# Kernel tuning notes

Measured on AMD Instinct MI355X. Metric: run time of the kernel, lower is better.

Reference implementation:

```python
import jax, jax.numpy as jnp
import numpy as np

H, CM, CS = 8, 16, 32  # num_heads, hidden_mv_channels, hidden_s_channels
_INNER_IDX = np.array([0, 2, 3, 4, 8, 9, 10, 14])  # PGA multivector components without e0


def _make_basis():
    # 9 Pin(3,0,1)-equivariant linear maps on 16-dim multivectors:
    # 5 grade projections + 4 left-multiplications by e0 (grade k -> grade k+1 e0-blades).
    # Component order: [1, e0, e1, e2, e3, e01, e02, e03, e12, e13, e23, e012, e013, e023, e123, e0123]
    b = np.zeros((9, 16, 16), dtype=np.float32)
    grades = [[0], [1, 2, 3, 4], [5, 6, 7, 8, 9, 10], [11, 12, 13, 14], [15]]
    for k, idxs in enumerate(grades):
        for i in idxs:
            b[k, i, i] = 1.0
    e0maps = {5: [(0, 1)], 6: [(2, 5), (3, 6), (4, 7)], 7: [(8, 11), (9, 12), (10, 13)], 8: [(14, 15)]}
    for k, pairs in e0maps.items():
        for i, o in pairs:
            b[k, o, i] = 1.0
    return jnp.asarray(b)


BASIS = _make_basis()  # (9, 16_out_comp, 16_in_comp)


def equi_linear(mv, s, w_mv, w_s2mv, b_mv, w_mv2s, w_s2s, b_s):
    # mv: (..., c_in, 16); s: (..., s_in)
    out_mv = jnp.einsum('yai,ocy,...ci->...oa', BASIS, w_mv, mv)
    out_mv = out_mv.at[..., 0].add(jnp.einsum('...i,oi->...o', s, w_s2mv) + b_mv)
    out_s = (jnp.einsum('...c,sc->...s', mv[..., 0], w_mv2s)
             + jnp.einsum('...i,si->...s', s, w_s2s) + b_s)
    return out_mv, out_s


def reference(multivectors_kv, multivectors_q, scalars_kv, scalars_q,
              q_w_mv, q_w_s2mv, q_b_mv, q_w_mv2s, q_w_s2s, q_b_s,
              k_w_mv, k_w_s2mv, k_b_mv, k_w_mv2s, k_w_s2s, k_b_s,
              v_w_mv, v_w_s2mv, v_b_mv, v_w_mv2s, v_w_s2s, v_b_s,
              o_w_mv, o_w_s2mv, o_b_mv, o_w_mv2s, o_w_s2s, o_b_s):
    B, Q = multivectors_q.shape[0], multivectors_q.shape[1]
    q_mv, q_s = equi_linear(multivectors_q, scalars_q, q_w_mv, q_w_s2mv, q_b_mv, q_w_mv2s, q_w_s2s, q_b_s)
    k_mv, k_s = equi_linear(multivectors_kv, scalars_kv, k_w_mv, k_w_s2mv, k_b_mv, k_w_mv2s, k_w_s2s, k_b_s)
    v_mv, v_s = equi_linear(multivectors_kv, scalars_kv, v_w_mv, v_w_s2mv, v_b_mv, v_w_mv2s, v_w_s2s, v_b_s)
    # split heads; einops pattern '(hidden_channels num_heads)' => channel-major, head-minor
    q_mv = q_mv.reshape(B, Q, CM, H, 16).transpose(0, 3, 1, 2, 4)  # (B,H,Q,CM,16)
    q_s = q_s.reshape(B, Q, CS, H).transpose(0, 3, 1, 2)            # (B,H,Q,CS)
    # multi-query: single k/v head broadcast over H
    scale = 1.0 / jnp.sqrt(jnp.asarray(8 * CM + CS, dtype=q_mv.dtype))
    scores = (jnp.einsum('bhqcx,bkcx->bhqk', q_mv[..., _INNER_IDX], k_mv[..., _INNER_IDX])
              + jnp.einsum('bhqs,bks->bhqk', q_s, k_s)) * scale
    attn = jax.nn.softmax(scores, axis=-1)
    h_mv = jnp.einsum('bhqk,bkcx->bhqcx', attn, v_mv)
    h_s = jnp.einsum('bhqk,bkc->bhqc', attn, v_s)
    # merge heads; pattern '(n_heads hidden_channels)' => head-major
    h_mv = h_mv.transpose(0, 2, 1, 3, 4).reshape(B, Q, H * CM, 16)
    h_s = h_s.transpose(0, 2, 1, 3).reshape(B, Q, H * CS)
    out_mv, out_s = equi_linear(h_mv, h_s, o_w_mv, o_w_s2mv, o_b_mv, o_w_mv2s, o_w_s2s, o_b_s)
    return out_mv, out_s


def setup_inputs():
    key = jax.random.key(0)
    ks = jax.random.split(key, 32)
    B, NQ, NKV, IN_MV, IN_S = 4, 2048, 2048, 16, 32
    w = 0.05  # weight scale to keep attention logits sane

    def rn(k, shape, s=1.0):
        return jax.random.normal(k, shape, dtype=jnp.float32) * s

    return {
        'multivectors_kv': rn(ks[0], (B, NKV, IN_MV, 16)),
        'multivectors_q': rn(ks[1], (B, NQ, IN_MV, 16)),
        'scalars_kv': rn(ks[2], (B, NKV, IN_S)),
        'scalars_q': rn(ks[3], (B, NQ, IN_S)),
        'q_w_mv': rn(ks[4], (CM * H, IN_MV, 9), w),
        'q_w_s2mv': rn(ks[5], (CM * H, IN_S), w),
        'q_b_mv': jnp.zeros((CM * H,), jnp.float32),
        'q_w_mv2s': rn(ks[6], (CS * H, IN_MV), w),
        'q_w_s2s': rn(ks[7], (CS * H, IN_S), w),
        'q_b_s': jnp.zeros((CS * H,), jnp.float32),
        'k_w_mv': rn(ks[8], (CM, IN_MV, 9), w),
        'k_w_s2mv': rn(ks[9], (CM, IN_S), w),
        'k_b_mv': jnp.zeros((CM,), jnp.float32),
        'k_w_mv2s': rn(ks[10], (CS, IN_MV), w),
        'k_w_s2s': rn(ks[11], (CS, IN_S), w),
        'k_b_s': jnp.zeros((CS,), jnp.float32),
        'v_w_mv': rn(ks[12], (CM, IN_MV, 9), w),
        'v_w_s2mv': rn(ks[13], (CM, IN_S), w),
        'v_b_mv': jnp.zeros((CM,), jnp.float32),
        'v_w_mv2s': rn(ks[14], (CS, IN_MV), w),
        'v_w_s2s': rn(ks[15], (CS, IN_S), w),
        'v_b_s': jnp.zeros((CS,), jnp.float32),
        'o_w_mv': rn(ks[16], (16, CM * H, 9), w),
        'o_w_s2mv': rn(ks[17], (16, CS * H), w),
        'o_b_mv': jnp.zeros((16,), jnp.float32),
        'o_w_mv2s': rn(ks[18], (32, CM * H), w),
        'o_w_s2s': rn(ks[19], (32, CS * H), w),
        'o_b_s': jnp.zeros((32,), jnp.float32),
    }
```

## Files before the change

### kernel.cpp

```cpp
#include <hip/hip_runtime.h>
#include <hip/hip_bf16.h>
#include <math.h>

#define NB   4
#define NQL  2048
#define NKVL 2048
#define HN   8
#define DQK  160
#define DV   288
#define QT   256
#define KTL  64
#define KLP  168

#define SCALE 0.07905694150420949f

typedef __attribute__((ext_vector_type(8)))  short short8;
typedef __attribute__((ext_vector_type(4)))  float f32x4;
typedef __attribute__((ext_vector_type(16))) float f32x16;

__constant__ int c_grade[16] = {0,1,1,1,1,2,2,2,2,2,2,3,3,3,3,4};
__constant__ int c_inner[8]  = {0,2,3,4,8,9,10,14};
__constant__ int c_esrc[16]  = {-1,0,-1,-1,-1,2,3,4,-1,-1,-1,8,9,10,-1,14};
__constant__ int c_ey[16]    = {0,5,0,0,0,6,6,6,0,0,0,7,7,7,0,8};

__device__ __forceinline__ ushort f2bf(float v) {
  __hip_bfloat16 h = __float2bfloat16(v);
  union { __hip_bfloat16 b; ushort u; } cv; cv.b = h; return cv.u;
}

__device__ __forceinline__ void gload16(const void* g, void* l) {
  __builtin_amdgcn_global_load_lds(
      (const __attribute__((address_space(1))) unsigned int*)g,
      (__attribute__((address_space(3))) unsigned int*)l, 16, 0, 0);
}

#define KWMV   0
#define KS2MV  2304
#define KMV2S  2816
#define KS2S   3328
#define KBMV   4352
#define KBS    4368
#define VWMV   4400
#define VS2MV  6704
#define VMV2S  7216
#define VS2S   7728
#define VBMV   8752
#define VBS    8768
#define WLSZ   8800
#define XSTR   289
#define OSTR   456
#define KVPOS  8

__device__ __forceinline__ void kv_accum(const float* wL, const float* xL,
                                         int f, float acc[KVPOS]) {
  if (f < 160) {
    if (f < 128) {
      int c = f >> 3, a = c_inner[f & 7], y = c_grade[a];
      float bias = (a == 0) ? wL[KBMV + c] : 0.f;
#pragma unroll
      for (int p = 0; p < KVPOS; p++) acc[p] = bias;
      for (int ci = 0; ci < 16; ci++) {
        float w = wL[KWMV + (c*16 + ci)*9 + y];
#pragma unroll
        for (int p = 0; p < KVPOS; p++) acc[p] += w * xL[p*XSTR + ci*16 + a];
      }
      if (a == 0) {
        for (int i2 = 0; i2 < 32; i2++) {
          float w = wL[KS2MV + c*32 + i2];
#pragma unroll
          for (int p = 0; p < KVPOS; p++) acc[p] += w * xL[p*XSTR + 256 + i2];
        }
      }
    } else {
      int si = f - 128;
      float bias = wL[KBS + si];
#pragma unroll
      for (int p = 0; p < KVPOS; p++) acc[p] = bias;
      for (int ci = 0; ci < 16; ci++) {
        float w = wL[KMV2S + si*16 + ci];
#pragma unroll
        for (int p = 0; p < KVPOS; p++) acc[p] += w * xL[p*XSTR + ci*16];
      }
      for (int i2 = 0; i2 < 32; i2++) {
        float w = wL[KS2S + si*32 + i2];
#pragma unroll
        for (int p = 0; p < KVPOS; p++) acc[p] += w * xL[p*XSTR + 256 + i2];
      }
    }
  } else {
    int g = f - 160;
    if (g < 256) {
      int c = g >> 4, a = g & 15, y = c_grade[a];
      float bias = (a == 0) ? wL[VBMV + c] : 0.f;
#pragma unroll
      for (int p = 0; p < KVPOS; p++) acc[p] = bias;
      for (int ci = 0; ci < 16; ci++) {
        float w = wL[VWMV + (c*16 + ci)*9 + y];
#pragma unroll
        for (int p = 0; p < KVPOS; p++) acc[p] += w * xL[p*XSTR + ci*16 + a];
      }
      int sa = c_esrc[a];
      if (sa >= 0) {
        int ey = c_ey[a];
        for (int ci = 0; ci < 16; ci++) {
          float w = wL[VWMV + (c*16 + ci)*9 + ey];
#pragma unroll
          for (int p = 0; p < KVPOS; p++) acc[p] += w * xL[p*XSTR + ci*16 + sa];
        }
      }
      if (a == 0) {
        for (int i2 = 0; i2 < 32; i2++) {
          float w = wL[VS2MV + c*32 + i2];
#pragma unroll
          for (int p = 0; p < KVPOS; p++) acc[p] += w * xL[p*XSTR + 256 + i2];
        }
      }
    } else {
      int si = g - 256;
      float bias = wL[VBS + si];
#pragma unroll
      for (int p = 0; p < KVPOS; p++) acc[p] = bias;
      for (int ci = 0; ci < 16; ci++) {
        float w = wL[VMV2S + si*16 + ci];
#pragma unroll
        for (int p = 0; p < KVPOS; p++) acc[p] += w * xL[p*XSTR + ci*16];
      }
      for (int i2 = 0; i2 < 32; i2++) {
        float w = wL[VS2S + si*32 + i2];
#pragma unroll
        for (int p = 0; p < KVPOS; p++) acc[p] += w * xL[p*XSTR + 256 + i2];
      }
    }
  }
}

__global__ __launch_bounds__(256) void proj_kv_kernel(
    const float* __restrict__ mv_kv, const float* __restrict__ s_kv,
    const float* __restrict__ kw_mv, const float* __restrict__ kw_s2mv, const float* __restrict__ kb_mv,
    const float* __restrict__ kw_mv2s, const float* __restrict__ kw_s2s, const float* __restrict__ kb_s,
    const float* __restrict__ vw_mv, const float* __restrict__ vw_s2mv, const float* __restrict__ vb_mv,
    const float* __restrict__ vw_mv2s, const float* __restrict__ vw_s2s, const float* __restrict__ vb_s,
    ushort* __restrict__ Kf, ushort* __restrict__ VfT)
{
  __shared__ float wL[WLSZ];
  __shared__ float xL[KVPOS*XSTR];
  int t = threadIdx.x;
  for (int i = t; i < 2304; i += 256) wL[KWMV + i] = kw_mv[i];
  for (int i = t; i < 512;  i += 256) wL[KS2MV + i] = kw_s2mv[i];
  for (int i = t; i < 512;  i += 256) wL[KMV2S + i] = kw_mv2s[i];
  for (int i = t; i < 1024; i += 256) wL[KS2S + i] = kw_s2s[i];
  if (t < 16) wL[KBMV + t] = kb_mv[t];
  if (t < 32) wL[KBS + t] = kb_s[t];
  for (int i = t; i < 2304; i += 256) wL[VWMV + i] = vw_mv[i];
  for (int i = t; i < 512;  i += 256) wL[VS2MV + i] = vw_s2mv[i];
  for (int i = t; i < 512;  i += 256) wL[VMV2S + i] = vw_mv2s[i];
  for (int i = t; i < 1024; i += 256) wL[VS2S + i] = vw_s2s[i];
  if (t < 16) wL[VBMV + t] = vb_mv[t];
  if (t < 32) wL[VBS + t] = vb_s[t];

  int p0 = blockIdx.x * KVPOS;
  for (int i = t; i < KVPOS*256; i += 256) {
    int p = i >> 8, c = i & 255;
    xL[p*XSTR + c] = mv_kv[(size_t)(p0 + p)*256 + c];
  }
  if (t < KVPOS*32) {
    int p = t >> 5, c = t & 31;
    xL[p*XSTR + 256 + c] = s_kv[(size_t)(p0 + p)*32 + c];
  }
  __syncthreads();

  float acc0[KVPOS], acc1[KVPOS];
  kv_accum(wL, xL, t, acc0);
  if (t < 192) kv_accum(wL, xL, 256 + t, acc1);
  __syncthreads();

  ushort* oL = (ushort*)xL;
#pragma unroll
  for (int p = 0; p < KVPOS; p++) oL[p*OSTR + t] = f2bf(acc0[p]);
  if (t < 192) {
#pragma unroll
    for (int p = 0; p < KVPOS; p++) oL[p*OSTR + 256 + t] = f2bf(acc1[p]);
  }
  __syncthreads();

  int b = p0 >> 11, kv0 = p0 & 2047;
  for (int it = 0; it < 3; it++) {
    int j = t + it*256;
    if (j < KVPOS*80) {
      int p = j / 80, fp = j - p*80;
      uint u = (uint)oL[p*OSTR + 2*fp] | ((uint)oL[p*OSTR + 2*fp + 1] << 16);
      *(uint*)(Kf + (size_t)(p0 + p)*DQK + 2*fp) = u;
    }
  }
  for (int it = 0; it < 5; it++) {
    int j = t + it*256;
    if (j < DV*(KVPOS/2)) {
      int g = j >> 2, pp = j & 3;
      uint u = (uint)oL[(2*pp)*OSTR + 160 + g] | ((uint)oL[(2*pp+1)*OSTR + 160 + g] << 16);
      int kv = kv0 + 2*pp;
      int pos = (kv & ~63) + ((((kv >> 3) & 7) ^ (g & 7)) << 3) + (kv & 7);
      *(uint*)(VfT + ((size_t)b*DV + g)*NKVL + pos) = u;
    }
  }
}

#define OWT_SZ 34816
#define QWT_MV 0
#define QWT_S  20480
#define QBT    61440
#define QWT_SZ 62720
__global__ __launch_bounds__(256) void prep_w_kernel(
    const float* __restrict__ ow_mv, const float* __restrict__ ow_s2mv,
    const float* __restrict__ ow_mv2s, const float* __restrict__ ow_s2s,
    float* __restrict__ owT,
    const float* __restrict__ qw_mv, const float* __restrict__ qw_s2mv, const float* __restrict__ qb_mv,
    const float* __restrict__ qw_mv2s, const float* __restrict__ qw_s2s, const float* __restrict__ qb_s,
    float* __restrict__ qwT)
{
  int i = blockIdx.x*256 + threadIdx.x;
  if (i < OWT_SZ) {
    if (i < 18432) {
      int y = i / 2048, r = i & 2047, ch = r >> 4, o = r & 15;
      owT[i] = ow_mv[(size_t)(o*128 + ch)*9 + y];
    } else if (i < 22528) {
      int r = i - 18432, jj = r >> 4, o = r & 15;
      owT[i] = ow_s2mv[o*256 + jj];
    } else if (i < 26624) {
      int r = i - 22528, ch = r >> 5, si = r & 31;
      owT[i] = ow_mv2s[si*128 + ch];
    } else {
      int r = i - 26624, jj = r >> 5, si = r & 31;
      owT[i] = ow_s2s[si*256 + jj];
    }
    return;
  }
  int j = i - OWT_SZ;
  if (j >= QWT_SZ) return;
  if (j < QWT_S) {
    int ci = j / 1280, r = j - ci*1280, h = r / 160, f0 = r - h*160;
    float v;
    if (f0 < 128) {
      int c = f0 >> 3, a = c_inner[f0 & 7], y = c_grade[a];
      v = qw_mv[((c*HN + h)*16 + ci)*9 + y];
    } else {
      v = qw_mv2s[((f0 - 128)*HN + h)*16 + ci];
    }
    qwT[j] = v;
  } else if (j < QBT) {
    int k = j - QWT_S;
    int i2 = k / 1280, r = k - i2*1280, h = r / 160, f0 = r - h*160;
    float v;
    if (f0 < 128) {
      int c = f0 >> 3, a = c_inner[f0 & 7];
      v = (a == 0) ? qw_s2mv[(c*HN + h)*32 + i2] : 0.f;
    } else {
      v = qw_s2s[((f0 - 128)*HN + h)*32 + i2];
    }
    qwT[j] = v;
  } else {
    int r = j - QBT, h = r / 160, f0 = r - h*160;
    float v;
    if (f0 < 128) {
      int c = f0 >> 3, a = c_inner[f0 & 7];
      v = (a == 0) ? qb_mv[c*HN + h] : 0.f;
    } else {
      v = qb_s[(f0 - 128)*HN + h];
    }
    qwT[j] = v;
  }
}

#define QPOS 8
__global__ __launch_bounds__(320) void proj_q_kernel(
    const float* __restrict__ mv_q, const float* __restrict__ s_q,
    const float* __restrict__ qwT,
    ushort* __restrict__ Qf)
{
  __shared__ float xL[QPOS*XSTR];
  int t = threadIdx.x;
  int p0 = blockIdx.x * QPOS;
  for (int i = t; i < QPOS*256; i += 320) {
    int p = i >> 8, c = i & 255;
    xL[p*XSTR + c] = mv_q[(size_t)(p0 + p)*256 + c];
  }
  if (t < QPOS*32) {
    int p = t >> 5, c = t & 31;
    xL[p*XSTR + 256 + c] = s_q[(size_t)(p0 + p)*32 + c];
  }
  __syncthreads();

  int f0 = t % 160;
  int h0 = t / 160;
  int a = (f0 < 128) ? c_inner[f0 & 7] : 0;

  float acc[4][QPOS];
#pragma unroll
  for (int k = 0; k < 4; k++) {
    float bv = qwT[QBT + (h0 + 2*k)*160 + f0];
#pragma unroll
    for (int p = 0; p < QPOS; p++) acc[k][p] = bv;
  }
  for (int ci = 0; ci < 16; ci++) {
    float w0 = qwT[QWT_MV + (ci*HN + h0    )*160 + f0];
    float w1 = qwT[QWT_MV + (ci*HN + h0 + 2)*160 + f0];
    float w2 = qwT[QWT_MV + (ci*HN + h0 + 4)*160 + f0];
    float w3 = qwT[QWT_MV + (ci*HN + h0 + 6)*160 + f0];
#pragma unroll
    for (int p = 0; p < QPOS; p++) {
      float xv = xL[p*XSTR + ci*16 + a];
      acc[0][p] += w0*xv; acc[1][p] += w1*xv;
      acc[2][p] += w2*xv; acc[3][p] += w3*xv;
    }
  }
  for (int i2 = 0; i2 < 32; i2++) {
    float w0 = qwT[QWT_S + (i2*HN + h0    )*160 + f0];
    float w1 = qwT[QWT_S + (i2*HN + h0 + 2)*160 + f0];
    float w2 = qwT[QWT_S + (i2*HN + h0 + 4)*160 + f0];
    float w3 = qwT[QWT_S + (i2*HN + h0 + 6)*160 + f0];
#pragma unroll
    for (int p = 0; p < QPOS; p++) {
      float xv = xL[p*XSTR + 256 + i2];
      acc[0][p] += w0*xv; acc[1][p] += w1*xv;
      acc[2][p] += w2*xv; acc[3][p] += w3*xv;
    }
  }

  int b = p0 >> 11, q0 = p0 & 2047;
#pragma unroll
  for (int k = 0; k < 4; k++) {
    int h = h0 + 2*k;
    ushort* qdst = Qf + ((size_t)(b*HN + h)*NQL + q0)*DQK + f0;
#pragma unroll
    for (int p = 0; p < QPOS; p++)
      qdst[p*DQK] = f2bf(acc[k][p] * SCALE);
  }
}

__global__ __launch_bounds__(512, 2) void attn_kernel(
    const ushort* __restrict__ Kf,
    const ushort* __restrict__ VfT,
    const ushort* __restrict__ Qf,
    float* __restrict__ Hf)
{
  __shared__ ushort kL[2][KTL*KLP];
  __shared__ ushort vtL[2][DV*KTL];

  const int NT = NQL/QT;
  int bid = blockIdx.x;
  int swz = (bid & 7) * 32 + (bid >> 3);
  int bh = swz / NT;
  int qt = swz - bh*NT;
  int b = bh >> 3, h = bh & 7;
  int t = threadIdx.x, w = t >> 6, l = t & 63;
  int ql = l & 31, hb = l >> 5;

  const ushort* kb = Kf  + (size_t)b*NKVL*DQK;
  const ushort* vb = VfT + (size_t)b*DV*NKVL;

  const ushort* qrow = Qf + ((size_t)bh*NQL + (size_t)qt*QT + w*32 + ql)*DQK + hb*8;
  short8 qf[10];
#pragma unroll
  for (int ks = 0; ks < 10; ks++)
    qf[ks] = *(const short8*)(qrow + ks*16);

  f32x16 oA[9];
#pragma unroll
  for (int i = 0; i < 9; i++) oA[i] = (f32x16)(0.f);
  float m = -INFINITY, lsum = 0.f;

#define STAGE(KT, BUF) do {                                            \
    const ushort* kg_ = kb + (size_t)(KT)*KTL*DQK;                     \
    char* kd_ = (char*)&kL[BUF][0];                                    \
    for (int c_ = w; c_ < 21; c_ += 8) {                               \
      int off_ = c_*1024 + l*16;                                       \
      int row_ = off_ / 336;                                           \
      int bc_  = off_ - row_*336;                                      \
      const ushort* ga_ = kg_ + row_*DQK + ((bc_ < 320) ? (bc_ >> 1) : 0); \
      gload16(ga_, kd_ + c_*1024);                                     \
    }                                                                  \
    const ushort* vg_ = vb + (size_t)(KT)*KTL;                         \
    char* vd_ = (char*)&vtL[BUF][0];                                   \
    for (int c_ = w; c_ < 36; c_ += 8) {                               \
      int off_ = c_*1024 + l*16;                                       \
      int d_  = off_ >> 7;                                             \
      int bc_ = off_ & 127;                                            \
      const ushort* ga_ = vg_ + (size_t)d_*NKVL + (bc_ >> 1);          \
      gload16(ga_, vd_ + c_*1024);                                     \
    }                                                                  \
  } while (0)

  STAGE(0, 0);
  __syncthreads();

  for (int kt = 0; kt < NKVL/KTL; kt++) {
    int cur = kt & 1;
    if (kt + 1 < NKVL/KTL) STAGE(kt + 1, cur ^ 1);

    const ushort* kbuf  = &kL[cur][0];
    const ushort* vtbuf = &vtL[cur][0];

    f32x16 sA[2];
    __builtin_amdgcn_s_setprio(1);
#pragma unroll
    for (int kvb = 0; kvb < 2; kvb++) {
      sA[kvb] = (f32x16)(0.f);
      const ushort* krow = kbuf + (ql + 32*kvb)*KLP + hb*8;
#pragma unroll
      for (int ks = 0; ks < 10; ks++) {
        short8 kf = *(const short8*)(krow + ks*16);
        sA[kvb] = __builtin_amdgcn_mfma_f32_32x32x16_bf16(kf, qf[ks], sA[kvb], 0, 0, 0);
      }
    }
    __builtin_amdgcn_s_setprio(0);

    float tm = sA[0][0];
#pragma unroll
    for (int kvb = 0; kvb < 2; kvb++)
#pragma unroll
      for (int r = 0; r < 16; r++) tm = fmaxf(tm, sA[kvb][r]);
    tm = fmaxf(tm, __shfl_xor(tm, 32));
    if (!__all(tm - m <= 8.0f)) {
      float nm = fmaxf(m, tm);
      float ef = __expf(m - nm);
      lsum *= ef;
#pragma unroll
      for (int i = 0; i < 9; i++)
#pragma unroll
        for (int r = 0; r < 16; r++) oA[i][r] *= ef;
      m = nm;
    }
    float rs = 0.f;
#pragma unroll
    for (int kvb = 0; kvb < 2; kvb++)
#pragma unroll
      for (int r = 0; r < 16; r++) {
        float p = __expf(sA[kvb][r] - m);
        sA[kvb][r] = p;
        rs += p;
      }
    rs += __shfl_xor(rs, 32);
    lsum += rs;

    unsigned int pk[2][8];
#pragma unroll
    for (int kvb = 0; kvb < 2; kvb++)
#pragma unroll
      for (int k = 0; k < 8; k++) {
        unsigned int r_;
        asm("v_cvt_pk_bf16_f32 %0, %1, %2" : "=v"(r_) : "v"(sA[kvb][2*k]), "v"(sA[kvb][2*k+1]));
        pk[kvb][k] = r_;
      }

#pragma unroll
    for (int s = 0; s < 4; s++) {
      const int n0 = 2*s, n1 = 2*s + 1;
      unsigned int u[4];
#pragma unroll
      for (int p = 0; p < 4; p++) {
        unsigned int Xa = pk[n0 >> 2][(p & 1) + 2*(n0 & 3)];
        unsigned int Xb = pk[n1 >> 2][(p & 1) + 2*(n1 & 3)];
        int src = ql + 32*(p >> 1);
        unsigned int ua = __shfl((int)Xa, src);
        unsigned int ub = __shfl((int)Xb, src);
        u[p] = hb ? ub : ua;
      }
      union { unsigned int uu[4]; short8 s8; } pf;
      pf.uu[0] = u[0]; pf.uu[1] = u[1]; pf.uu[2] = u[2]; pf.uu[3] = u[3];
      __builtin_amdgcn_s_setprio(1);
#pragma unroll
      for (int db = 0; db < 9; db++) {
        int d = ql + 32*db;
        int col = (((2*s + hb) ^ (d & 7)) << 3);
        short8 vf = *(const short8*)(vtbuf + d*KTL + col);
        oA[db] = __builtin_amdgcn_mfma_f32_32x32x16_bf16(vf, pf.s8, oA[db], 0, 0, 0);
      }
      __builtin_amdgcn_s_setprio(0);
    }
    __syncthreads();
  }
#undef STAGE

  float inv = 1.0f / lsum;
  int q = qt*QT + w*32 + ql;
  float* orow = Hf + (((size_t)b*NQL + q)*HN + h)*DV;
#pragma unroll
  for (int db = 0; db < 9; db++)
#pragma unroll
    for (int j = 0; j < 4; j++) {
      int d0 = 32*db + 8*j + 4*hb;
      float4 st = make_float4(oA[db][4*j]*inv, oA[db][4*j+1]*inv,
                              oA[db][4*j+2]*inv, oA[db][4*j+3]*inv);
      *(float4*)(orow + d0) = st;
    }
}

#define HSTR 2308
#define OPOS 4
__global__ __launch_bounds__(256) void proj_o_kernel(
    const float* __restrict__ Hf,
    const float* __restrict__ owT,
    const float* __restrict__ ob_mv, const float* __restrict__ ob_s,
    float* __restrict__ outp)
{
  __shared__ float hL[OPOS*HSTR];
  __shared__ float pL[128*8];
  __shared__ float sP[128];
  int t = threadIdx.x;
  int p0 = blockIdx.x * OPOS;
  for (int i = t; i < OPOS*2304/4; i += 256) {
    int idx = i*4; int p = idx / 2304; int c = idx - p*2304;
    *(float4*)(hL + p*HSTR + c) = *(const float4*)(Hf + (size_t)(p0 + p)*2304 + c);
  }
  __syncthreads();

  const float* mvT   = owT;
  const float* s2mvT = owT + 18432;
  const float* mv2sT = owT + 22528;
  const float* s2sT  = owT + 26624;

  int o = t & 15, pp = (t >> 4) & 3, half = (t >> 6) & 1, seg = t >> 7;
  const float* x = hL + pp*HSTR;
  float acc[8];
#pragma unroll
  for (int a = 0; a < 8; a++) acc[a] = 0.f;
  if (half == 0 && seg == 0) acc[0] = ob_mv[o];
  int ch0 = seg*64;

  if (half == 0) {
    for (int ch = ch0; ch < ch0 + 64; ch++) {
      const float* xc = x + (ch >> 4)*288 + (ch & 15)*16;
      float w0 = mvT[0*2048 + ch*16 + o], w1 = mvT[1*2048 + ch*16 + o];
      float w2 = mvT[2*2048 + ch*16 + o];
      float w5 = mvT[5*2048 + ch*16 + o], w6 = mvT[6*2048 + ch*16 + o];
      float x0 = xc[0], x1 = xc[1], x2 = xc[2], x3 = xc[3];
      float x4 = xc[4], x5 = xc[5], x6 = xc[6], x7 = xc[7];
      acc[0] += w0*x0;
      acc[1] += w1*x1 + w5*x0;
      acc[2] += w1*x2;
      acc[3] += w1*x3;
      acc[4] += w1*x4;
      acc[5] += w2*x5 + w6*x2;
      acc[6] += w2*x6 + w6*x3;
      acc[7] += w2*x7 + w6*x4;
    }
    for (int jj = seg*128; jj < seg*128 + 128; jj++)
      acc[0] += s2mvT[jj*16 + o] * x[(jj >> 5)*288 + 256 + (jj & 31)];
  } else {
    for (int ch = ch0; ch < ch0 + 64; ch++) {
      const float* xc = x + (ch >> 4)*288 + (ch & 15)*16 + 8;
      float w2 = mvT[2*2048 + ch*16 + o], w3 = mvT[3*2048 + ch*16 + o];
      float w4 = mvT[4*2048 + ch*16 + o];
      float w7 = mvT[7*2048 + ch*16 + o], w8 = mvT[8*2048 + ch*16 + o];
      float x8 = xc[0], x9 = xc[1], x10 = xc[2], x11 = xc[3];
      float x12 = xc[4], x13 = xc[5], x14 = xc[6], x15 = xc[7];
      acc[0] += w2*x8;
      acc[1] += w2*x9;
      acc[2] += w2*x10;
      acc[3] += w3*x11 + w7*x8;
      acc[4] += w3*x12 + w7*x9;
      acc[5] += w3*x13 + w7*x10;
      acc[6] += w3*x14;
      acc[7] += w4*x15 + w8*x14;
    }
  }

  int si = t & 31, ps = (t >> 5) & 3;
  const float* xs = hL + ps*HSTR;
  float vs = (seg == 0) ? ob_s[si] : 0.f;
  for (int ch = seg*64; ch < seg*64 + 64; ch++)
    vs += mv2sT[ch*32 + si] * xs[(ch >> 4)*288 + (ch & 15)*16];
  for (int jj = seg*128; jj < seg*128 + 128; jj++)
    vs += s2sT[jj*32 + si] * xs[(jj >> 5)*288 + 256 + (jj & 31)];

  if (seg == 1) {
    float* pd = pL + ((half*4 + pp)*16 + o)*8;
#pragma unroll
    for (int a = 0; a < 8; a++) pd[a] = acc[a];
    sP[ps*32 + si] = vs;
  }
  __syncthreads();
  if (seg == 0) {
    const float* pd = pL + ((half*4 + pp)*16 + o)*8;
#pragma unroll
    for (int a = 0; a < 8; a++) acc[a] += pd[a];
    float* od = outp + (size_t)(p0 + pp)*256 + o*16 + half*8;
    *(float4*)(od)     = make_float4(acc[0], acc[1], acc[2], acc[3]);
    *(float4*)(od + 4) = make_float4(acc[4], acc[5], acc[6], acc[7]);
    vs += sP[ps*32 + si];
    float* out_s = outp + (size_t)NB*NQL*256;
    out_s[(size_t)(p0 + ps)*32 + si] = vs;
  }
}

extern "C" void kernel_launch(void* const* d_in, const int* in_sizes, int n_in,
                              void* d_out, int out_size, void* d_ws, size_t ws_size,
                              hipStream_t stream)
{
  const float* mv_kv = (const float*)d_in[0];
  const float* mv_q  = (const float*)d_in[1];
  const float* s_kv  = (const float*)d_in[2];
  const float* s_q   = (const float*)d_in[3];

  ushort* Kf  = (ushort*)d_ws;
  ushort* VfT = Kf  + (size_t)NB*NKVL*DQK;
  ushort* Qf  = VfT + (size_t)NB*DV*NKVL;
  float*  Hf  = (float*)(Qf + (size_t)NB*HN*NQL*DQK);
  float*  owT = Hf + (size_t)NB*NQL*HN*DV;
  float*  qwT = owT + OWT_SZ;

  prep_w_kernel<<<(OWT_SZ + QWT_SZ + 255)/256, 256, 0, stream>>>(
      (const float*)d_in[22], (const float*)d_in[23],
      (const float*)d_in[25], (const float*)d_in[26], owT,
      (const float*)d_in[4], (const float*)d_in[5], (const float*)d_in[6],
      (const float*)d_in[7], (const float*)d_in[8], (const float*)d_in[9],
      qwT);
  proj_kv_kernel<<<NB*NKVL/KVPOS, 256, 0, stream>>>(mv_kv, s_kv,
      (const float*)d_in[10], (const float*)d_in[11], (const float*)d_in[12],
      (const float*)d_in[13], (const float*)d_in[14], (const float*)d_in[15],
      (const float*)d_in[16], (const float*)d_in[17], (const float*)d_in[18],
      (const float*)d_in[19], (const float*)d_in[20], (const float*)d_in[21],
      Kf, VfT);
  proj_q_kernel<<<NB*NQL/QPOS, 320, 0, stream>>>(mv_q, s_q, qwT, Qf);
  attn_kernel<<<NB*HN*(NQL/QT), 512, 0, stream>>>(Kf, VfT, Qf, Hf);
  proj_o_kernel<<<NB*NQL/OPOS, 256, 0, stream>>>(Hf, owT,
      (const float*)d_in[24], (const float*)d_in[27],
      (float*)d_out);
}
```

Baseline: 385.7 us.

## Restructure output projection to reuse weights across eight positions per block

The output projection kernel now handles eight positions per block with 512 threads instead of four with 256. Each thread owns one (output channel, component) pair and loads each weight once, reusing it across all eight positions instead of reloading it per position. The scalar paths are split across eight channel segments and reduced through shared memory, with staged, coalesced output writes. In exchange the block uses about twice the shared memory, which may lower occupancy, and adds an extra barrier and reduction step.

```diff
diff --git a/kernel.cpp b/kernel.cpp
--- a/kernel.cpp
+++ b/kernel.cpp
@@ -494,22 +494,22 @@
     }
 }
 
-#define HSTR 2308
-#define OPOS 4
-__global__ __launch_bounds__(256) void proj_o_kernel(
+#define HSTR2 2308
+#define OPOS2 8
+__global__ __launch_bounds__(512) void proj_o_kernel(
     const float* __restrict__ Hf,
     const float* __restrict__ owT,
     const float* __restrict__ ob_mv, const float* __restrict__ ob_s,
     float* __restrict__ outp)
 {
-  __shared__ float hL[OPOS*HSTR];
-  __shared__ float pL[128*8];
-  __shared__ float sP[128];
+  __shared__ float hL[OPOS2*HSTR2];
+  __shared__ float pL[256*8];
+  __shared__ float sP[8*48*8];
   int t = threadIdx.x;
-  int p0 = blockIdx.x * OPOS;
-  for (int i = t; i < OPOS*2304/4; i += 256) {
+  int p0 = blockIdx.x * OPOS2;
+  for (int i = t; i < OPOS2*2304/4; i += 512) {
     int idx = i*4; int p = idx / 2304; int c = idx - p*2304;
-    *(float4*)(hL + p*HSTR + c) = *(const float4*)(Hf + (size_t)(p0 + p)*2304 + c);
+    *(float4*)(hL + p*HSTR2 + c) = *(const float4*)(Hf + (size_t)(p0 + p)*2304 + c);
   }
   __syncthreads();
 
@@ -518,77 +518,96 @@
   const float* mv2sT = owT + 22528;
   const float* s2sT  = owT + 26624;
 
-  int o = t & 15, pp = (t >> 4) & 3, half = (t >> 6) & 1, seg = t >> 7;
-  const float* x = hL + pp*HSTR;
-  float acc[8];
-#pragma unroll
-  for (int a = 0; a < 8; a++) acc[a] = 0.f;
-  if (half == 0 && seg == 0) acc[0] = ob_mv[o];
-  int ch0 = seg*64;
-
-  if (half == 0) {
-    for (int ch = ch0; ch < ch0 + 64; ch++) {
-      const float* xc = x + (ch >> 4)*288 + (ch & 15)*16;
-      float w0 = mvT[0*2048 + ch*16 + o], w1 = mvT[1*2048 + ch*16 + o];
-      float w2 = mvT[2*2048 + ch*16 + o];
-      float w5 = mvT[5*2048 + ch*16 + o], w6 = mvT[6*2048 + ch*16 + o];
-      float x0 = xc[0], x1 = xc[1], x2 = xc[2], x3 = xc[3];
-      float x4 = xc[4], x5 = xc[5], x6 = xc[6], x7 = xc[7];
-      acc[0] += w0*x0;
-      acc[1] += w1*x1 + w5*x0;
-      acc[2] += w1*x2;
-      acc[3] += w1*x3;
-      acc[4] += w1*x4;
-      acc[5] += w2*x5 + w6*x2;
-      acc[6] += w2*x6 + w6*x3;
-      acc[7] += w2*x7 + w6*x4;
-    }
-    for (int jj = seg*128; jj < seg*128 + 128; jj++)
-      acc[0] += s2mvT[jj*16 + o] * x[(jj >> 5)*288 + 256 + (jj & 31)];
-  } else {
-    for (int ch = ch0; ch < ch0 + 64; ch++) {
-      const float* xc = x + (ch >> 4)*288 + (ch & 15)*16 + 8;
-      float w2 = mvT[2*2048 + ch*16 + o], w3 = mvT[3*2048 + ch*16 + o];
-      float w4 = mvT[4*2048 + ch*16 + o];
-      float w7 = mvT[7*2048 + ch*16 + o], w8 = mvT[8*2048 + ch*16 + o];
-      float x8 = xc[0], x9 = xc[1], x10 = xc[2], x11 = xc[3];
-      float x12 = xc[4], x13 = xc[5], x14 = xc[6], x15 = xc[7];
-      acc[0] += w2*x8;
-      acc[1] += w2*x9;
-      acc[2] += w2*x10;
-      acc[3] += w3*x11 + w7*x8;
-      acc[4] += w3*x12 + w7*x9;
-      acc[5] += w3*x13 + w7*x10;
-      acc[6] += w3*x14;
-      acc[7] += w4*x15 + w8*x14;
-    }
-  }
-
-  int si = t & 31, ps = (t >> 5) & 3;
-  const float* xs = hL + ps*HSTR;
-  float vs = (seg == 0) ? ob_s[si] : 0.f;
-  for (int ch = seg*64; ch < seg*64 + 64; ch++)
-    vs += mv2sT[ch*32 + si] * xs[(ch >> 4)*288 + (ch & 15)*16];
-  for (int jj = seg*128; jj < seg*128 + 128; jj++)
-    vs += s2sT[jj*32 + si] * xs[(jj >> 5)*288 + 256 + (jj & 31)];
-
+  int o = t & 15, a = (t >> 4) & 15, seg = t >> 8;
+  int oa = o*16 + a;
+  int y = c_grade[a], sa = c_esrc[a], ey = c_ey[a];
+  float acc[OPOS2];
+#pragma unroll
+  for (int p = 0; p < OPOS2; p++) acc[p] = 0.f;
+  for (int ch = seg*64; ch < seg*64 + 64; ch++) {
+    int xb = (ch >> 4)*288 + (ch & 15)*16;
+    float w1 = mvT[y*2048 + ch*16 + o];
+#pragma unroll
+    for (int p = 0; p < OPOS2; p++) acc[p] += w1 * hL[p*HSTR2 + xb + a];
+    if (sa >= 0) {
+      float w2 = mvT[ey*2048 + ch*16 + o];
+#pragma unroll
+      for (int p = 0; p < OPOS2; p++) acc[p] += w2 * hL[p*HSTR2 + xb + sa];
+    }
+  }
   if (seg == 1) {
-    float* pd = pL + ((half*4 + pp)*16 + o)*8;
-#pragma unroll
-    for (int a = 0; a < 8; a++) pd[a] = acc[a];
-    sP[ps*32 + si] = vs;
+#pragma unroll
+    for (int p = 0; p < OPOS2; p++) pL[oa*8 + p] = acc[p];
   }
   __syncthreads();
   if (seg == 0) {
-    const float* pd = pL + ((half*4 + pp)*16 + o)*8;
-#pragma unroll
-    for (int a = 0; a < 8; a++) acc[a] += pd[a];
-    float* od = outp + (size_t)(p0 + pp)*256 + o*16 + half*8;
-    *(float4*)(od)     = make_float4(acc[0], acc[1], acc[2], acc[3]);
-    *(float4*)(od + 4) = make_float4(acc[4], acc[5], acc[6], acc[7]);
-    vs += sP[ps*32 + si];
+#pragma unroll
+    for (int p = 0; p < OPOS2; p++) acc[p] += pL[oa*8 + p];
+  }
+
+  int v = t >> 6, u = t & 63;
+  float sacc[OPOS2];
+#pragma unroll
+  for (int p = 0; p < OPOS2; p++) sacc[p] = 0.f;
+  if (u < 32) {
+    int si = u;
+    for (int ch = v*16; ch < v*16 + 16; ch++) {
+      float w = mv2sT[ch*32 + si];
+      int xb = (ch >> 4)*288 + (ch & 15)*16;
+#pragma unroll
+      for (int p = 0; p < OPOS2; p++) sacc[p] += w * hL[p*HSTR2 + xb];
+    }
+    for (int jj = v*32; jj < v*32 + 32; jj++) {
+      float w = s2sT[jj*32 + si];
+      int xb = (jj >> 5)*288 + 256 + (jj & 31);
+#pragma unroll
+      for (int p = 0; p < OPOS2; p++) sacc[p] += w * hL[p*HSTR2 + xb];
+    }
+  } else if (u < 48) {
+    int o2 = u - 32;
+    for (int jj = v*32; jj < v*32 + 32; jj++) {
+      float w = s2mvT[jj*16 + o2];
+      int xb = (jj >> 5)*288 + 256 + (jj & 31);
+#pragma unroll
+      for (int p = 0; p < OPOS2; p++) sacc[p] += w * hL[p*HSTR2 + xb];
+    }
+  }
+  if (u < 48) {
+#pragma unroll
+    for (int p = 0; p < OPOS2; p++) sP[(v*48 + u)*8 + p] = sacc[p];
+  }
+  __syncthreads();
+
+  if (seg == 0) {
+    if (a == 0) {
+      float bv = ob_mv[o];
+#pragma unroll
+      for (int p = 0; p < OPOS2; p++) {
+        float s = bv;
+#pragma unroll
+        for (int vv = 0; vv < 8; vv++) s += sP[(vv*48 + 32 + o)*8 + p];
+        acc[p] += s;
+      }
+    }
+#pragma unroll
+    for (int p = 0; p < OPOS2; p++) pL[oa*8 + p] = acc[p];
+  }
+  __syncthreads();
+  for (int i = t; i < 256*OPOS2; i += 512) {
+    int p = i >> 8, c = i & 255;
+    outp[(size_t)(p0 + p)*256 + c] = pL[c*8 + p];
+  }
+  if (t >= 256 && t < 256 + 32) {
+    int si = t - 256;
+    float bv = ob_s[si];
     float* out_s = outp + (size_t)NB*NQL*256;
-    out_s[(size_t)(p0 + ps)*32 + si] = vs;
+#pragma unroll
+    for (int p = 0; p < OPOS2; p++) {
+      float s = bv;
+#pragma unroll
+      for (int vv = 0; vv < 8; vv++) s += sP[(vv*48 + si)*8 + p];
+      out_s[(size_t)(p0 + p)*32 + si] = s;
+    }
   }
 }
 
@@ -622,7 +641,7 @@
       Kf, VfT);
   proj_q_kernel<<<NB*NQL/QPOS, 320, 0, stream>>>(mv_q, s_q, qwT, Qf);
   attn_kernel<<<NB*HN*(NQL/QT), 512, 0, stream>>>(Kf, VfT, Qf, Hf);
-  proj_o_kernel<<<NB*NQL/OPOS, 256, 0, stream>>>(Hf, owT,
+  proj_o_kernel<<<NB*NQL/OPOS2, 512, 0, stream>>>(Hf, owT,
       (const float*)d_in[24], (const float*)d_in[27],
       (float*)d_out);
 }
```

Result: faster. 335.2 us (-13.1%).
